# Performance work log

Hardware: AMD Instinct MI355X
Metric: run time of the kernel (lower is better)

Reference implementation:

```python
import jax, jax.numpy as jnp
import numpy as np

DIM = 384
H_RES, W_RES = 56, 56
HEADS = 12
WS = 7          # window size
SS = 3          # shift size
N = WS * WS     # tokens per window
NW = (H_RES // WS) * (W_RES // WS)
EPS = 1e-5


def _rel_pos_index(ws):
    coords = np.stack(np.meshgrid(np.arange(ws), np.arange(ws), indexing='ij'))  # [2,ws,ws]
    cf = coords.reshape(2, -1)                      # [2, N]
    rc = (cf[:, :, None] - cf[:, None, :]).transpose(1, 2, 0)  # [N,N,2]
    rc[..., 0] += ws - 1
    rc[..., 1] += ws - 1
    rc[..., 0] *= 2 * ws - 1
    return rc.sum(-1)                               # [N,N] int


def _attn_mask(h, w, ws, ss):
    img = np.zeros((h, w))
    cnt = 0
    slices = (slice(0, -ws), slice(-ws, -ss), slice(-ss, None))
    for hs in slices:
        for wsl in slices:
            img[hs, wsl] = cnt
            cnt += 1
    mw = img.reshape(h // ws, ws, w // ws, ws).transpose(0, 2, 1, 3).reshape(-1, ws * ws)  # [nW,N]
    d = mw[:, None, :] - mw[:, :, None]
    return np.where(d != 0, -100.0, 0.0).astype(np.float32)  # [nW,N,N]


RPI = jnp.asarray(_rel_pos_index(WS).reshape(-1))          # [N*N]
ATTN_MASK = jnp.asarray(_attn_mask(H_RES, W_RES, WS, SS))  # [nW,N,N]


def _layernorm(x, g, b):
    mu = jnp.mean(x, axis=-1, keepdims=True)
    var = jnp.mean(jnp.square(x - mu), axis=-1, keepdims=True)
    return (x - mu) * jax.lax.rsqrt(var + EPS) * g + b


def setup_inputs() -> dict:
    key = jax.random.key(0)
    ks = jax.random.split(key, 8)
    s = 0.02
    return {
        'x': jax.random.normal(ks[0], (32, 1 + H_RES * W_RES, DIM), jnp.float32),
        'norm1_g': jnp.ones((DIM,), jnp.float32),
        'norm1_b': jnp.zeros((DIM,), jnp.float32),
        'qkv_w': jax.random.normal(ks[1], (DIM, 3 * DIM), jnp.float32) * s,
        'qkv_b': jnp.zeros((3 * DIM,), jnp.float32),
        'rpb_table': jax.random.normal(ks[2], ((2 * WS - 1) ** 2, HEADS), jnp.float32) * s,
        'proj_w': jax.random.normal(ks[3], (DIM, DIM), jnp.float32) * s,
        'proj_b': jnp.zeros((DIM,), jnp.float32),
        'norm2_g': jnp.ones((DIM,), jnp.float32),
        'norm2_b': jnp.zeros((DIM,), jnp.float32),
        'fc1_w': jax.random.normal(ks[4], (DIM, 4 * DIM), jnp.float32) * s,
        'fc1_b': jnp.zeros((4 * DIM,), jnp.float32),
        'fc2_w': jax.random.normal(ks[5], (4 * DIM, DIM), jnp.float32) * s,
        'fc2_b': jnp.zeros((DIM,), jnp.float32),
    }


def reference(x, norm1_g, norm1_b, qkv_w, qkv_b, rpb_table, proj_w, proj_b,
              norm2_g, norm2_b, fc1_w, fc1_b, fc2_w, fc2_b):
    B = x.shape[0]
    C = DIM
    hd = C // HEADS
    scale = hd ** -0.5

    time_token = x[:, :1, :]          # [B,1,C]
    img = x[:, 1:, :]                 # [B,H*W,C]
    shortcut = img

    h = _layernorm(img, norm1_g, norm1_b).reshape(B, H_RES, W_RES, C)
    h = jnp.roll(h, shift=(-SS, -SS), axis=(1, 2))  # cyclic shift

    # window partition -> [B*nW, N, C]
    xw = h.reshape(B, H_RES // WS, WS, W_RES // WS, WS, C)
    xw = xw.transpose(0, 1, 3, 2, 4, 5).reshape(-1, N, C)

    # window attention
    qkv = (xw @ qkv_w + qkv_b).reshape(-1, N, 3, HEADS, hd).transpose(2, 0, 3, 1, 4)
    q, k, v = qkv[0], qkv[1], qkv[2]                 # [B*nW, H, N, hd]
    attn = jnp.einsum('whnd,whmd->whnm', q * scale, k)
    bias = rpb_table[RPI].reshape(N, N, HEADS).transpose(2, 0, 1)  # [H,N,N]
    attn = attn + bias[None]
    attn = attn.reshape(B, NW, HEADS, N, N) + ATTN_MASK[None, :, None]
    attn = jax.nn.softmax(attn.reshape(-1, HEADS, N, N), axis=-1)
    out = jnp.einsum('whnm,whmd->wnhd', attn, v).reshape(-1, N, C)
    out = out @ proj_w + proj_b

    # window reverse -> [B,H,W,C]
    out = out.reshape(B, H_RES // WS, W_RES // WS, WS, WS, C)
    out = out.transpose(0, 1, 3, 2, 4, 5).reshape(B, H_RES, W_RES, C)
    out = jnp.roll(out, shift=(SS, SS), axis=(1, 2)).reshape(B, H_RES * W_RES, C)

    img = shortcut + out
    x = jnp.concatenate([time_token, img], axis=1)   # [B,1+H*W,C]
    x = _layernorm(x, norm2_g, norm2_b)
    hmlp = jax.nn.gelu(x @ fc1_w + fc1_b, approximate=False)
    x = x + (hmlp @ fc2_w + fc2_b)
    return x
```

## Files before the change

kernel.cpp:

```cpp
#include <hip/hip_runtime.h>
#include <hip/hip_bf16.h>

#define DIM 384
#define HEADS 12
#define NTOK 49
#define TOKENS 3137
#define M_ATTN 100352
#define M_FULL 100384
#define M_PAD  100480
#define SCALEQ 0.17677669529663687f

typedef __attribute__((ext_vector_type(8))) short s8v;
typedef __attribute__((ext_vector_type(4))) float f4v;
typedef unsigned short u16;

__device__ __forceinline__ float b2f(int s) {
  union { unsigned u; float f; } c; c.u = ((unsigned)(s & 0xffff)) << 16; return c.f;
}
__device__ __forceinline__ u16 f2b(float f) {
  __hip_bfloat16 h = __float2bfloat16(f);
  return *reinterpret_cast<u16*>(&h);
}
__device__ __forceinline__ void gload16(const void* g, void* l) {
  __builtin_amdgcn_global_load_lds((const __attribute__((address_space(1))) void*)g,
                                   (__attribute__((address_space(3))) void*)l, 16, 0, 0);
}
__device__ __forceinline__ float gelu_f(float val) {
  float u = __builtin_fmaf(0.0713548163f * val, val * val, 1.5957691216f * val);
  return val * __builtin_amdgcn_rcpf(1.0f + __expf(-u));
}

__global__ void k_convert(const float* __restrict__ qkv_w, const float* __restrict__ qkv_b,
                          const float* __restrict__ proj_w, const float* __restrict__ fc1_w,
                          const float* __restrict__ fc2_w,
                          u16* __restrict__ wt_qkv, float* __restrict__ qkvb_s,
                          u16* __restrict__ wt_proj, u16* __restrict__ wt_fc1,
                          u16* __restrict__ wt_fc2) {
  int i = blockIdx.x * 256 + threadIdx.x;
  if (i < 1152 * 384) { int n = i / 384, k = i % 384;
    float v = qkv_w[(size_t)k * 1152 + n]; if (n < 384) v *= SCALEQ; wt_qkv[i] = f2b(v); }
  if (i < 1152) qkvb_s[i] = qkv_b[i] * (i < 384 ? SCALEQ : 1.0f);
  if (i < 384 * 384) { int n = i / 384, k = i % 384; wt_proj[i] = f2b(proj_w[(size_t)k * 384 + n]); }
  if (i < 1536 * 384) { int n = i / 384, k = i % 384; wt_fc1[i] = f2b(fc1_w[(size_t)k * 1536 + n]); }
  if (i < 384 * 1536) { int n = i / 1536, k = i % 1536; wt_fc2[i] = f2b(fc2_w[(size_t)k * 384 + n]); }
}

__global__ void k_addtab(const float* __restrict__ rpb, float* __restrict__ ADD) {
  int idx = blockIdx.x * 256 + threadIdx.x;
  if (idx >= 4 * HEADS * NTOK * NTOK) return;
  int j = idx % NTOK, t = idx / NTOK;
  int i = t % NTOK; t /= NTOK;
  int h = t % HEADS; int cls = t / HEADS;
  int ii = i / 7, jj = i % 7, ji = j / 7, j2 = j % 7;
  int rpi = (ii - ji + 6) * 13 + (jj - j2 + 6);
  float v = rpb[rpi * HEADS + h];
  int rh = (cls & 2) ? (ii < 4 ? 1 : 2) : 0;
  int rw = (cls & 1) ? (jj < 4 ? 1 : 2) : 0;
  int sh = (cls & 2) ? (ji < 4 ? 1 : 2) : 0;
  int sw = (cls & 1) ? (j2 < 4 ? 1 : 2) : 0;
  if (rh != sh || rw != sw) v -= 100.0f;
  ADD[idx] = v;
}

__global__ void k_ln1(const float* __restrict__ x, const float* __restrict__ g,
                      const float* __restrict__ b, u16* __restrict__ xw, int t0) {
  int wid = threadIdx.x >> 6, lane = threadIdx.x & 63;
  int t = t0 + blockIdx.x * 4 + wid;
  int bi = t / 3136, rem = t % 3136;
  int win = rem / NTOK, n = rem % NTOK;
  int wh = win >> 3, ww = win & 7, ii = n / 7, jj = n % 7;
  int h = (wh * 7 + ii + 3) % 56;
  int w = (ww * 7 + jj + 3) % 56;
  const float* src = x + ((size_t)bi * TOKENS + 1 + h * 56 + w) * DIM;
  float v[6];
  #pragma unroll
  for (int e = 0; e < 6; e++) v[e] = src[lane + e * 64];
  float s = v[0] + v[1] + v[2] + v[3] + v[4] + v[5];
  #pragma unroll
  for (int m = 1; m < 64; m <<= 1) s += __shfl_xor(s, m);
  float mu = s * (1.0f / 384.0f);
  float q = 0.f;
  #pragma unroll
  for (int e = 0; e < 6; e++) { float d = v[e] - mu; q += d * d; }
  #pragma unroll
  for (int m = 1; m < 64; m <<= 1) q += __shfl_xor(q, m);
  float rstd = rsqrtf(q * (1.0f / 384.0f) + 1e-5f);
  u16* dst = xw + (size_t)(t - t0) * DIM;
  #pragma unroll
  for (int e = 0; e < 6; e++) {
    int c = lane + e * 64;
    dst[c] = f2b((v[e] - mu) * rstd * g[c] + b[c]);
  }
}

template<int MODE>
__global__ __launch_bounds__(512, 1) void k_panel(
    const u16* __restrict__ A, const u16* __restrict__ Wa, const u16* __restrict__ Wb,
    const float* __restrict__ ba, const float* __restrict__ bb,
    u16* __restrict__ outb, float* __restrict__ outf, int N) {
  __shared__ __align__(16) u16 Xs[128 * 384];
  __shared__ __align__(16) u16 Ws[128 * 64];
  __shared__ __align__(16) u16 Hs[(MODE == 1) ? 128 * 128 : 16];
  int tid = threadIdx.x;
  int wid = tid >> 6, lane = tid & 63, lo = lane & 15, hi = lane >> 4;
  int mh = (wid >> 2) * 64;
  int nq = (wid & 3) * 32;
  int m0 = blockIdx.x * 128;
  const u16* Ap = A + (size_t)m0 * 384;

  #pragma unroll
  for (int i = 0; i < 12; i++) {
    int f = (wid * 12 + i) * 1024 + lane * 16;
    int row = f / 768;
    int slot = (f - row * 768) >> 4;
    gload16(Ap + row * 384 + ((slot ^ (row & 7)) << 3),
            (char*)Xs + (wid * 12 + i) * 1024);
  }

  auto stageW = [&](const u16* Wt, int Krow, int rowbase, int kc) {
    #pragma unroll
    for (int i = 0; i < 2; i++) {
      int f = (wid * 2 + i) * 1024 + lane * 16;
      int row = f >> 7;
      int slot = (f >> 4) & 7;
      gload16(Wt + (size_t)(rowbase + row) * Krow + kc + ((slot ^ (row & 7)) << 3),
              (char*)Ws + (wid * 2 + i) * 1024);
    }
  };

  if (MODE == 0) {
    int nch = N >> 7;
    for (int ch = 0; ch < nch; ch++) {
      f4v acc[4][2];
      #pragma unroll
      for (int mi = 0; mi < 4; mi++)
        #pragma unroll
        for (int ni = 0; ni < 2; ni++) acc[mi][ni] = (f4v)(0.0f);
      for (int ks = 0; ks < 6; ks++) {
        __syncthreads();
        stageW(Wa, 384, ch * 128, ks * 64);
        asm volatile("s_waitcnt vmcnt(0)" ::: "memory");
        __syncthreads();
        #pragma unroll
        for (int kk = 0; kk < 2; kk++) {
          s8v a[4], b[2];
          #pragma unroll
          for (int mi = 0; mi < 4; mi++) {
            int m = mh + mi * 16 + lo; int s = (ks * 2 + kk) * 4 + hi;
            a[mi] = *(const s8v*)(Xs + m * 384 + ((s ^ (m & 7)) << 3));
          }
          #pragma unroll
          for (int ni = 0; ni < 2; ni++) {
            int nr = nq + ni * 16 + lo; int s = kk * 4 + hi;
            b[ni] = *(const s8v*)(Ws + nr * 64 + ((s ^ (nr & 7)) << 3));
          }
          #pragma unroll
          for (int mi = 0; mi < 4; mi++)
            #pragma unroll
            for (int ni = 0; ni < 2; ni++)
              acc[mi][ni] = __builtin_amdgcn_mfma_f32_16x16x32_bf16(a[mi], b[ni], acc[mi][ni], 0, 0, 0);
        }
      }
      #pragma unroll
      for (int mi = 0; mi < 4; mi++)
        #pragma unroll
        for (int ni = 0; ni < 2; ni++) {
          int gcol = ch * 128 + nq + ni * 16 + lo;
          float bv = ba[gcol];
          #pragma unroll
          for (int r = 0; r < 4; r++) {
            int grow = mh + mi * 16 + hi * 4 + r;
            outb[(size_t)(m0 + grow) * N + gcol] = f2b(acc[mi][ni][r] + bv);
          }
        }
    }
  } else {
    f4v acc2[3][4][2];
    #pragma unroll
    for (int g = 0; g < 3; g++)
      #pragma unroll
      for (int mi = 0; mi < 4; mi++)
        #pragma unroll
        for (int ni = 0; ni < 2; ni++) acc2[g][mi][ni] = (f4v)(0.0f);
    for (int ch = 0; ch < 12; ch++) {
      f4v acc1[4][2];
      #pragma unroll
      for (int mi = 0; mi < 4; mi++)
        #pragma unroll
        for (int ni = 0; ni < 2; ni++) acc1[mi][ni] = (f4v)(0.0f);
      for (int ks = 0; ks < 6; ks++) {
        __syncthreads();
        stageW(Wa, 384, ch * 128, ks * 64);
        asm volatile("s_waitcnt vmcnt(0)" ::: "memory");
        __syncthreads();
        #pragma unroll
        for (int kk = 0; kk < 2; kk++) {
          s8v a[4], b[2];
          #pragma unroll
          for (int mi = 0; mi < 4; mi++) {
            int m = mh + mi * 16 + lo; int s = (ks * 2 + kk) * 4 + hi;
            a[mi] = *(const s8v*)(Xs + m * 384 + ((s ^ (m & 7)) << 3));
          }
          #pragma unroll
          for (int ni = 0; ni < 2; ni++) {
            int nr = nq + ni * 16 + lo; int s = kk * 4 + hi;
            b[ni] = *(const s8v*)(Ws + nr * 64 + ((s ^ (nr & 7)) << 3));
          }
          #pragma unroll
          for (int mi = 0; mi < 4; mi++)
            #pragma unroll
            for (int ni = 0; ni < 2; ni++)
              acc1[mi][ni] = __builtin_amdgcn_mfma_f32_16x16x32_bf16(a[mi], b[ni], acc1[mi][ni], 0, 0, 0);
        }
      }
      #pragma unroll
      for (int mi = 0; mi < 4; mi++)
        #pragma unroll
        for (int ni = 0; ni < 2; ni++) {
          int col = nq + ni * 16 + lo;
          float bv = ba[ch * 128 + col];
          int sl = col >> 3, el = col & 7;
          #pragma unroll
          for (int r = 0; r < 4; r++) {
            int m = mh + mi * 16 + hi * 4 + r;
            Hs[m * 128 + ((sl ^ (m & 7)) << 3) + el] = f2b(gelu_f(acc1[mi][ni][r] + bv));
          }
        }
      #pragma unroll
      for (int n2g = 0; n2g < 3; n2g++)
        for (int kt2 = 0; kt2 < 2; kt2++) {
          __syncthreads();
          stageW(Wb, 1536, n2g * 128, ch * 128 + kt2 * 64);
          asm volatile("s_waitcnt vmcnt(0)" ::: "memory");
          __syncthreads();
          #pragma unroll
          for (int kk = 0; kk < 2; kk++) {
            s8v a[4], b[2];
            #pragma unroll
            for (int mi = 0; mi < 4; mi++) {
              int m = mh + mi * 16 + lo; int s = (kt2 * 2 + kk) * 4 + hi;
              a[mi] = *(const s8v*)(Hs + m * 128 + ((s ^ (m & 7)) << 3));
            }
            #pragma unroll
            for (int ni = 0; ni < 2; ni++) {
              int nr = nq + ni * 16 + lo; int s = kk * 4 + hi;
              b[ni] = *(const s8v*)(Ws + nr * 64 + ((s ^ (nr & 7)) << 3));
            }
            #pragma unroll
            for (int mi = 0; mi < 4; mi++)
              #pragma unroll
              for (int ni = 0; ni < 2; ni++)
                acc2[n2g][mi][ni] = __builtin_amdgcn_mfma_f32_16x16x32_bf16(a[mi], b[ni], acc2[n2g][mi][ni], 0, 0, 0);
          }
        }
    }
    #pragma unroll
    for (int n2g = 0; n2g < 3; n2g++)
      #pragma unroll
      for (int mi = 0; mi < 4; mi++)
        #pragma unroll
        for (int ni = 0; ni < 2; ni++) {
          int gcol = n2g * 128 + nq + ni * 16 + lo;
          float bv = bb[gcol];
          int sl = gcol >> 3, el = gcol & 7;
          #pragma unroll
          for (int r = 0; r < 4; r++) {
            int ml = mh + mi * 16 + hi * 4 + r;
            int orow = m0 + ml;
            if (orow < M_FULL) {
              float res = b2f(Xs[ml * 384 + ((sl ^ (ml & 7)) << 3) + el]);
              outf[(size_t)orow * 384 + gcol] = acc2[n2g][mi][ni][r] + bv + res;
            }
          }
        }
  }
}

__global__ __launch_bounds__(256) void k_attn2(const u16* __restrict__ qkv,
                                               const float* __restrict__ ADD,
                                               u16* __restrict__ ao, int win0) {
  __shared__ u16 PT[4][64][76];
  __shared__ u16 VT[4][32][76];
  int wid = threadIdx.x >> 6, lane = threadIdx.x & 63;
  int lo = lane & 15, hi = lane >> 4;
  int win_l = blockIdx.x * 4 + wid;
  int nw = (win0 + win_l) & 63;
  int wh = nw >> 3, ww = nw & 7;
  int cls = ((wh == 7) ? 2 : 0) + ((ww == 7) ? 1 : 0);
  size_t rowbase = (size_t)win_l * NTOK;
  u16 (*pt)[76] = PT[wid];
  u16 (*vt)[76] = VT[wid];

  int rcl[4];
  #pragma unroll
  for (int ti = 0; ti < 4; ti++) {
    int r = ti * 16 + lo;
    rcl[ti] = r < NTOK ? r : NTOK - 1;
  }
  int jrow = lane < NTOK ? lane : NTOK - 1;

  for (int h = 0; h < HEADS; h++) {
    s8v af[4], bf[4];
    #pragma unroll
    for (int ti = 0; ti < 4; ti++) {
      af[ti] = *(const s8v*)(qkv + (rowbase + rcl[ti]) * 1152 + h * 32 + hi * 8);
      bf[ti] = *(const s8v*)(qkv + (rowbase + rcl[ti]) * 1152 + 384 + h * 32 + hi * 8);
    }
    f4v st[4][4];
    #pragma unroll
    for (int mi = 0; mi < 4; mi++)
      #pragma unroll
      for (int ni = 0; ni < 4; ni++)
        st[mi][ni] = __builtin_amdgcn_mfma_f32_16x16x32_bf16(af[mi], bf[ni], (f4v)(0.0f), 0, 0, 0);

    {
      const u16* vsrc = qkv + (rowbase + jrow) * 1152 + 768 + h * 32;
      #pragma unroll
      for (int d0 = 0; d0 < 32; d0 += 8) {
        s8v v = *(const s8v*)(vsrc + d0);
        #pragma unroll
        for (int e = 0; e < 8; e++) vt[d0 + e][lane] = (u16)v[e];
      }
    }

    const float* addb = ADD + ((size_t)cls * HEADS + h) * (NTOK * NTOK);
    #pragma unroll
    for (int mi = 0; mi < 4; mi++)
      #pragma unroll
      for (int ni = 0; ni < 4; ni++) {
        int jj = ni * 16 + lo;
        #pragma unroll
        for (int r = 0; r < 4; r++) {
          int i = mi * 16 + hi * 4 + r;
          if (jj < NTOK) {
            int ic = i < NTOK ? i : NTOK - 1;
            st[mi][ni][r] += addb[ic * NTOK + jj];
          } else st[mi][ni][r] = -1e30f;
        }
      }

    float invl[4][4];
    #pragma unroll
    for (int mi = 0; mi < 4; mi++)
      #pragma unroll
      for (int r = 0; r < 4; r++) {
        float m = fmaxf(fmaxf(st[mi][0][r], st[mi][1][r]), fmaxf(st[mi][2][r], st[mi][3][r]));
        #pragma unroll
        for (int msk = 1; msk < 16; msk <<= 1) m = fmaxf(m, __shfl_xor(m, msk));
        float s = 0.f;
        #pragma unroll
        for (int ni = 0; ni < 4; ni++) {
          float p = __expf(st[mi][ni][r] - m);
          st[mi][ni][r] = p;
          s += p;
        }
        #pragma unroll
        for (int msk = 1; msk < 16; msk <<= 1) s += __shfl_xor(s, msk);
        invl[mi][r] = 1.0f / s;
      }

    #pragma unroll
    for (int ni = 0; ni < 4; ni++)
      #pragma unroll
      for (int mi = 0; mi < 4; mi++) {
        ushort4 pk;
        pk.x = f2b(st[mi][ni][0]); pk.y = f2b(st[mi][ni][1]);
        pk.z = f2b(st[mi][ni][2]); pk.w = f2b(st[mi][ni][3]);
        *(ushort4*)(&pt[ni * 16 + lo][mi * 16 + hi * 4]) = pk;
      }

    f4v ot[4][2];
    #pragma unroll
    for (int mi = 0; mi < 4; mi++)
      #pragma unroll
      for (int dt = 0; dt < 2; dt++) ot[mi][dt] = (f4v)(0.0f);
    #pragma unroll
    for (int kt = 0; kt < 2; kt++) {
      s8v pa[4], vb[2];
      #pragma unroll
      for (int mi = 0; mi < 4; mi++) {
        s8v p;
        #pragma unroll
        for (int e = 0; e < 8; e++) p[e] = (short)pt[kt * 32 + hi * 8 + e][mi * 16 + lo];
        pa[mi] = p;
      }
      #pragma unroll
      for (int dt = 0; dt < 2; dt++) {
        short4 a = *(const short4*)(&vt[dt * 16 + lo][kt * 32 + hi * 8]);
        short4 b = *(const short4*)(&vt[dt * 16 + lo][kt * 32 + hi * 8 + 4]);
        s8v v; v[0] = a.x; v[1] = a.y; v[2] = a.z; v[3] = a.w;
               v[4] = b.x; v[5] = b.y; v[6] = b.z; v[7] = b.w;
        vb[dt] = v;
      }
      #pragma unroll
      for (int mi = 0; mi < 4; mi++)
        #pragma unroll
        for (int dt = 0; dt < 2; dt++)
          ot[mi][dt] = __builtin_amdgcn_mfma_f32_16x16x32_bf16(pa[mi], vb[dt], ot[mi][dt], 0, 0, 0);
    }

    #pragma unroll
    for (int mi = 0; mi < 4; mi++)
      #pragma unroll
      for (int r = 0; r < 4; r++) {
        int i = mi * 16 + hi * 4 + r;
        if (i < NTOK) {
          u16* op = ao + (rowbase + i) * DIM + h * 32 + lo;
          op[0]  = f2b(ot[mi][0][r] * invl[mi][r]);
          op[16] = f2b(ot[mi][1][r] * invl[mi][r]);
        }
      }
  }
}

__global__ void k_ln2(const float* __restrict__ x, const u16* __restrict__ proj,
                      const float* __restrict__ g, const float* __restrict__ b,
                      u16* __restrict__ x2b) {
  int wid = threadIdx.x >> 6, lane = threadIdx.x & 63;
  int r = blockIdx.x * 4 + wid;
  u16* dst = x2b + (size_t)r * DIM;
  if (r >= M_FULL) {
    u16 z = f2b(0.0f);
    #pragma unroll
    for (int e = 0; e < 6; e++) dst[lane + e * 64] = z;
    return;
  }
  int bi = r / TOKENS, tk = r % TOKENS;
  const float* xs = x + (size_t)r * DIM;
  float v[6];
  if (tk == 0) {
    #pragma unroll
    for (int e = 0; e < 6; e++) v[e] = xs[lane + e * 64];
  } else {
    int p = tk - 1, hh = p / 56, wp = p % 56;
    int a = (hh + 53) % 56, bw = (wp + 53) % 56;
    int wh = a / 7, ii = a % 7, w2 = bw / 7, jj = bw % 7;
    size_t prow = ((size_t)bi * 64 + wh * 8 + w2) * NTOK + ii * 7 + jj;
    const u16* ps = proj + prow * DIM;
    #pragma unroll
    for (int e = 0; e < 6; e++) v[e] = xs[lane + e * 64] + b2f(ps[lane + e * 64]);
  }
  float s = v[0] + v[1] + v[2] + v[3] + v[4] + v[5];
  #pragma unroll
  for (int m = 1; m < 64; m <<= 1) s += __shfl_xor(s, m);
  float mu = s * (1.0f / 384.0f);
  float q = 0.f;
  #pragma unroll
  for (int e = 0; e < 6; e++) { float d = v[e] - mu; q += d * d; }
  #pragma unroll
  for (int m = 1; m < 64; m <<= 1) q += __shfl_xor(q, m);
  float rstd = rsqrtf(q * (1.0f / 384.0f) + 1e-5f);
  #pragma unroll
  for (int e = 0; e < 6; e++) {
    int c = lane + e * 64;
    dst[c] = f2b((v[e] - mu) * rstd * g[c] + b[c]);
  }
}

extern "C" void kernel_launch(void* const* d_in, const int* in_sizes, int n_in,
                              void* d_out, int out_size, void* d_ws, size_t ws_size,
                              hipStream_t stream) {
  const float* x      = (const float*)d_in[0];
  const float* n1g    = (const float*)d_in[1];
  const float* n1b    = (const float*)d_in[2];
  const float* qkv_w  = (const float*)d_in[3];
  const float* qkv_b  = (const float*)d_in[4];
  const float* rpb    = (const float*)d_in[5];
  const float* proj_w = (const float*)d_in[6];
  const float* proj_b = (const float*)d_in[7];
  const float* n2g    = (const float*)d_in[8];
  const float* n2b    = (const float*)d_in[9];
  const float* fc1_w  = (const float*)d_in[10];
  const float* fc1_b  = (const float*)d_in[11];
  const float* fc2_w  = (const float*)d_in[12];
  const float* fc2_b  = (const float*)d_in[13];
  float* outp = (float*)d_out;

  auto al = [](size_t v) { return (v + 255) & ~(size_t)255; };
  size_t fixed = al(884736) + al(294912) + al(1179648) + al(1179648) + al(4608)
               + al(460992) + al((size_t)M_ATTN * 768) + al((size_t)M_PAD * 768);
  const int cands[5] = {1, 2, 4, 8, 16};
  int NC1 = 16;
  for (int ci = 0; ci < 5; ci++) {
    int c1 = cands[ci];
    size_t tot = fixed + al((size_t)(M_ATTN / c1) * 768) + al((size_t)(M_ATTN / c1) * 2304);
    if (tot <= ws_size) { NC1 = c1; break; }
  }
  char* p = (char*)d_ws;
  auto take = [&](size_t bytes) { char* r = p; p += al(bytes); return r; };
  u16* wt_qkv  = (u16*)take(884736);
  u16* wt_proj = (u16*)take(294912);
  u16* wt_fc1  = (u16*)take(1179648);
  u16* wt_fc2  = (u16*)take(1179648);
  float* qkvb_s = (float*)take(4608);
  float* ADDt   = (float*)take(460992);
  u16* PROJ = (u16*)take((size_t)M_ATTN * 768);
  u16* X2B  = (u16*)take((size_t)M_PAD * 768);
  int chunkM = M_ATTN / NC1;
  u16* XW   = (u16*)take((size_t)chunkM * 768);
  u16* QKV  = (u16*)take((size_t)chunkM * 2304);
  u16* AO = XW;

  k_convert<<<2304, 256, 0, stream>>>(qkv_w, qkv_b, proj_w, fc1_w, fc2_w,
                                      wt_qkv, qkvb_s, wt_proj, wt_fc1, wt_fc2);
  k_addtab<<<451, 256, 0, stream>>>(rpb, ADDt);
  int chunkWin = chunkM / NTOK;
  for (int c = 0; c < NC1; c++) {
    int t0 = c * chunkM;
    k_ln1<<<chunkM / 4, 256, 0, stream>>>(x, n1g, n1b, XW, t0);
    k_panel<0><<<chunkM / 128, 512, 0, stream>>>(XW, wt_qkv, nullptr, qkvb_s, nullptr,
                                                 QKV, nullptr, 1152);
    k_attn2<<<chunkWin / 4, 256, 0, stream>>>(QKV, ADDt, AO, c * chunkWin);
    k_panel<0><<<chunkM / 128, 512, 0, stream>>>(AO, wt_proj, nullptr, proj_b, nullptr,
                                                 PROJ + (size_t)t0 * DIM, nullptr, 384);
  }
  k_ln2<<<M_PAD / 4, 256, 0, stream>>>(x, PROJ, n2g, n2b, X2B);
  k_panel<1><<<M_PAD / 128, 512, 0, stream>>>(X2B, wt_fc1, wt_fc2, fc1_b, fc2_b,
                                              nullptr, outp, 384);
}
```

Baseline: 1.258 ms.

## Load GEMM weight fragments directly from global memory and shrink QKV/proj tiles

The panel GEMM no longer stages weight tiles through LDS with a barrier pair per k-step. Each wave now loads its B fragments straight from global memory (relying on cache), and only the activation panel stays in LDS. The QKV and projection launches switch to 64-row blocks of 4 waves with a higher occupancy hint, so more blocks fit per CU. The risk is uncoalesced, repeated weight reads from L2 in place of shared LDS reuse across waves, plus extra register pressure.

```diff
diff --git a/kernel.cpp b/kernel.cpp
--- a/kernel.cpp
+++ b/kernel.cpp
@@ -93,72 +93,56 @@
   }
 }
 
-template<int MODE>
-__global__ __launch_bounds__(512, 1) void k_panel(
+template<int MODE, int MR, int NWAVE>
+__global__ __launch_bounds__(NWAVE * 64, MODE == 0 ? 3 : 2) void k_panel(
     const u16* __restrict__ A, const u16* __restrict__ Wa, const u16* __restrict__ Wb,
     const float* __restrict__ ba, const float* __restrict__ bb,
     u16* __restrict__ outb, float* __restrict__ outf, int N) {
-  __shared__ __align__(16) u16 Xs[128 * 384];
-  __shared__ __align__(16) u16 Ws[128 * 64];
-  __shared__ __align__(16) u16 Hs[(MODE == 1) ? 128 * 128 : 16];
+  __shared__ __align__(16) u16 Xs[MR * 384];
+  __shared__ __align__(16) u16 Hs[(MODE == 1) ? MR * 128 : 16];
   int tid = threadIdx.x;
   int wid = tid >> 6, lane = tid & 63, lo = lane & 15, hi = lane >> 4;
-  int mh = (wid >> 2) * 64;
-  int nq = (wid & 3) * 32;
-  int m0 = blockIdx.x * 128;
+  int mh = (MR == 128) ? (wid >> 2) * 64 : 0;
+  int nq = (MR == 128 ? (wid & 3) : wid) * 32;
+  int m0 = blockIdx.x * MR;
   const u16* Ap = A + (size_t)m0 * 384;
 
   #pragma unroll
   for (int i = 0; i < 12; i++) {
-    int f = (wid * 12 + i) * 1024 + lane * 16;
+    int base = (wid * 12 + i) * 1024;
+    int f = base + lane * 16;
     int row = f / 768;
     int slot = (f - row * 768) >> 4;
-    gload16(Ap + row * 384 + ((slot ^ (row & 7)) << 3),
-            (char*)Xs + (wid * 12 + i) * 1024);
-  }
-
-  auto stageW = [&](const u16* Wt, int Krow, int rowbase, int kc) {
-    #pragma unroll
-    for (int i = 0; i < 2; i++) {
-      int f = (wid * 2 + i) * 1024 + lane * 16;
-      int row = f >> 7;
-      int slot = (f >> 4) & 7;
-      gload16(Wt + (size_t)(rowbase + row) * Krow + kc + ((slot ^ (row & 7)) << 3),
-              (char*)Ws + (wid * 2 + i) * 1024);
-    }
+    gload16(Ap + row * 384 + ((slot ^ (row & 7)) << 3), (char*)Xs + base);
+  }
+  asm volatile("s_waitcnt vmcnt(0)" ::: "memory");
+  __syncthreads();
+
+  auto ldsA = [&](int m, int s) -> s8v {
+    return *(const s8v*)(Xs + m * 384 + ((s ^ (m & 7)) << 3));
   };
 
   if (MODE == 0) {
     int nch = N >> 7;
     for (int ch = 0; ch < nch; ch++) {
+      const u16* W0 = Wa + (size_t)(ch * 128 + nq + lo) * 384;
+      const u16* W1 = Wa + (size_t)(ch * 128 + nq + 16 + lo) * 384;
       f4v acc[4][2];
       #pragma unroll
       for (int mi = 0; mi < 4; mi++)
         #pragma unroll
         for (int ni = 0; ni < 2; ni++) acc[mi][ni] = (f4v)(0.0f);
-      for (int ks = 0; ks < 6; ks++) {
-        __syncthreads();
-        stageW(Wa, 384, ch * 128, ks * 64);
-        asm volatile("s_waitcnt vmcnt(0)" ::: "memory");
-        __syncthreads();
-        #pragma unroll
-        for (int kk = 0; kk < 2; kk++) {
-          s8v a[4], b[2];
-          #pragma unroll
-          for (int mi = 0; mi < 4; mi++) {
-            int m = mh + mi * 16 + lo; int s = (ks * 2 + kk) * 4 + hi;
-            a[mi] = *(const s8v*)(Xs + m * 384 + ((s ^ (m & 7)) << 3));
-          }
-          #pragma unroll
-          for (int ni = 0; ni < 2; ni++) {
-            int nr = nq + ni * 16 + lo; int s = kk * 4 + hi;
-            b[ni] = *(const s8v*)(Ws + nr * 64 + ((s ^ (nr & 7)) << 3));
-          }
-          #pragma unroll
-          for (int mi = 0; mi < 4; mi++)
-            #pragma unroll
-            for (int ni = 0; ni < 2; ni++)
-              acc[mi][ni] = __builtin_amdgcn_mfma_f32_16x16x32_bf16(a[mi], b[ni], acc[mi][ni], 0, 0, 0);
+      #pragma unroll
+      for (int kt = 0; kt < 12; kt++) {
+        s8v b0 = *(const s8v*)(W0 + kt * 32 + hi * 8);
+        s8v b1 = *(const s8v*)(W1 + kt * 32 + hi * 8);
+        s8v a[4];
+        #pragma unroll
+        for (int mi = 0; mi < 4; mi++) a[mi] = ldsA(mi * 16 + lo, kt * 4 + hi);
+        #pragma unroll
+        for (int mi = 0; mi < 4; mi++) {
+          acc[mi][0] = __builtin_amdgcn_mfma_f32_16x16x32_bf16(a[mi], b0, acc[mi][0], 0, 0, 0);
+          acc[mi][1] = __builtin_amdgcn_mfma_f32_16x16x32_bf16(a[mi], b1, acc[mi][1], 0, 0, 0);
         }
       }
       #pragma unroll
@@ -169,7 +153,7 @@
           float bv = ba[gcol];
           #pragma unroll
           for (int r = 0; r < 4; r++) {
-            int grow = mh + mi * 16 + hi * 4 + r;
+            int grow = mi * 16 + hi * 4 + r;
             outb[(size_t)(m0 + grow) * N + gcol] = f2b(acc[mi][ni][r] + bv);
           }
         }
@@ -183,36 +167,27 @@
         #pragma unroll
         for (int ni = 0; ni < 2; ni++) acc2[g][mi][ni] = (f4v)(0.0f);
     for (int ch = 0; ch < 12; ch++) {
+      const u16* W0 = Wa + (size_t)(ch * 128 + nq + lo) * 384;
+      const u16* W1 = Wa + (size_t)(ch * 128 + nq + 16 + lo) * 384;
       f4v acc1[4][2];
       #pragma unroll
       for (int mi = 0; mi < 4; mi++)
         #pragma unroll
         for (int ni = 0; ni < 2; ni++) acc1[mi][ni] = (f4v)(0.0f);
-      for (int ks = 0; ks < 6; ks++) {
-        __syncthreads();
-        stageW(Wa, 384, ch * 128, ks * 64);
-        asm volatile("s_waitcnt vmcnt(0)" ::: "memory");
-        __syncthreads();
-        #pragma unroll
-        for (int kk = 0; kk < 2; kk++) {
-          s8v a[4], b[2];
-          #pragma unroll
-          for (int mi = 0; mi < 4; mi++) {
-            int m = mh + mi * 16 + lo; int s = (ks * 2 + kk) * 4 + hi;
-            a[mi] = *(const s8v*)(Xs + m * 384 + ((s ^ (m & 7)) << 3));
-          }
-          #pragma unroll
-          for (int ni = 0; ni < 2; ni++) {
-            int nr = nq + ni * 16 + lo; int s = kk * 4 + hi;
-            b[ni] = *(const s8v*)(Ws + nr * 64 + ((s ^ (nr & 7)) << 3));
-          }
-          #pragma unroll
-          for (int mi = 0; mi < 4; mi++)
-            #pragma unroll
-            for (int ni = 0; ni < 2; ni++)
-              acc1[mi][ni] = __builtin_amdgcn_mfma_f32_16x16x32_bf16(a[mi], b[ni], acc1[mi][ni], 0, 0, 0);
-        }
-      }
+      #pragma unroll
+      for (int kt = 0; kt < 12; kt++) {
+        s8v b0 = *(const s8v*)(W0 + kt * 32 + hi * 8);
+        s8v b1 = *(const s8v*)(W1 + kt * 32 + hi * 8);
+        s8v a[4];
+        #pragma unroll
+        for (int mi = 0; mi < 4; mi++) a[mi] = ldsA(mh + mi * 16 + lo, kt * 4 + hi);
+        #pragma unroll
+        for (int mi = 0; mi < 4; mi++) {
+          acc1[mi][0] = __builtin_amdgcn_mfma_f32_16x16x32_bf16(a[mi], b0, acc1[mi][0], 0, 0, 0);
+          acc1[mi][1] = __builtin_amdgcn_mfma_f32_16x16x32_bf16(a[mi], b1, acc1[mi][1], 0, 0, 0);
+        }
+      }
+      __syncthreads();
       #pragma unroll
       for (int mi = 0; mi < 4; mi++)
         #pragma unroll
@@ -226,33 +201,29 @@
             Hs[m * 128 + ((sl ^ (m & 7)) << 3) + el] = f2b(gelu_f(acc1[mi][ni][r] + bv));
           }
         }
-      #pragma unroll
-      for (int n2g = 0; n2g < 3; n2g++)
-        for (int kt2 = 0; kt2 < 2; kt2++) {
-          __syncthreads();
-          stageW(Wb, 1536, n2g * 128, ch * 128 + kt2 * 64);
-          asm volatile("s_waitcnt vmcnt(0)" ::: "memory");
-          __syncthreads();
+      __syncthreads();
+      #pragma unroll
+      for (int n2g = 0; n2g < 3; n2g++) {
+        const u16* V0 = Wb + (size_t)(n2g * 128 + nq + lo) * 1536 + ch * 128;
+        const u16* V1 = Wb + (size_t)(n2g * 128 + nq + 16 + lo) * 1536 + ch * 128;
+        #pragma unroll
+        for (int kt = 0; kt < 4; kt++) {
+          s8v b0 = *(const s8v*)(V0 + kt * 32 + hi * 8);
+          s8v b1 = *(const s8v*)(V1 + kt * 32 + hi * 8);
+          s8v a[4];
           #pragma unroll
-          for (int kk = 0; kk < 2; kk++) {
-            s8v a[4], b[2];
-            #pragma unroll
-            for (int mi = 0; mi < 4; mi++) {
-              int m = mh + mi * 16 + lo; int s = (kt2 * 2 + kk) * 4 + hi;
-              a[mi] = *(const s8v*)(Hs + m * 128 + ((s ^ (m & 7)) << 3));
-            }
-            #pragma unroll
-            for (int ni = 0; ni < 2; ni++) {
-              int nr = nq + ni * 16 + lo; int s = kk * 4 + hi;
-              b[ni] = *(const s8v*)(Ws + nr * 64 + ((s ^ (nr & 7)) << 3));
-            }
-            #pragma unroll
-            for (int mi = 0; mi < 4; mi++)
-              #pragma unroll
-              for (int ni = 0; ni < 2; ni++)
-                acc2[n2g][mi][ni] = __builtin_amdgcn_mfma_f32_16x16x32_bf16(a[mi], b[ni], acc2[n2g][mi][ni], 0, 0, 0);
+          for (int mi = 0; mi < 4; mi++) {
+            int m = mh + mi * 16 + lo;
+            int s = kt * 4 + hi;
+            a[mi] = *(const s8v*)(Hs + m * 128 + ((s ^ (m & 7)) << 3));
           }
-        }
+          #pragma unroll
+          for (int mi = 0; mi < 4; mi++) {
+            acc2[n2g][mi][0] = __builtin_amdgcn_mfma_f32_16x16x32_bf16(a[mi], b0, acc2[n2g][mi][0], 0, 0, 0);
+            acc2[n2g][mi][1] = __builtin_amdgcn_mfma_f32_16x16x32_bf16(a[mi], b1, acc2[n2g][mi][1], 0, 0, 0);
+          }
+        }
+      }
     }
     #pragma unroll
     for (int n2g = 0; n2g < 3; n2g++)
@@ -508,13 +479,14 @@
   for (int c = 0; c < NC1; c++) {
     int t0 = c * chunkM;
     k_ln1<<<chunkM / 4, 256, 0, stream>>>(x, n1g, n1b, XW, t0);
-    k_panel<0><<<chunkM / 128, 512, 0, stream>>>(XW, wt_qkv, nullptr, qkvb_s, nullptr,
-                                                 QKV, nullptr, 1152);
+    k_panel<0, 64, 4><<<chunkM / 64, 256, 0, stream>>>(XW, wt_qkv, nullptr, qkvb_s,
+                                                       nullptr, QKV, nullptr, 1152);
     k_attn2<<<chunkWin / 4, 256, 0, stream>>>(QKV, ADDt, AO, c * chunkWin);
-    k_panel<0><<<chunkM / 128, 512, 0, stream>>>(AO, wt_proj, nullptr, proj_b, nullptr,
-                                                 PROJ + (size_t)t0 * DIM, nullptr, 384);
+    k_panel<0, 64, 4><<<chunkM / 64, 256, 0, stream>>>(AO, wt_proj, nullptr, proj_b,
+                                                       nullptr, PROJ + (size_t)t0 * DIM,
+                                                       nullptr, 384);
   }
   k_ln2<<<M_PAD / 4, 256, 0, stream>>>(x, PROJ, n2g, n2b, X2B);
-  k_panel<1><<<M_PAD / 128, 512, 0, stream>>>(X2B, wt_fc1, wt_fc2, fc1_b, fc2_b,
-                                              nullptr, outp, 384);
-}
+  k_panel<1, 128, 8><<<M_PAD / 128, 512, 0, stream>>>(X2B, wt_fc1, wt_fc2, fc1_b, fc2_b,
+                                                      nullptr, outp, 384);
+}
```

Result: slower. 1.632 ms (+29.7%).
